# Performance work log

Measured on AMD Instinct MI355X. Metric: run time of the kernel, lower is better.

## Reference

```python
import jax, jax.numpy as jnp
import numpy as np

B, S, D, H = 8, 1024, 1024, 16
HD = D // H  # head_size = 64


def layernorm(x, g, b, eps=1e-5):
    mu = jnp.mean(x, axis=-1, keepdims=True)
    var = jnp.var(x, axis=-1, keepdims=True)
    return (x - mu) * jax.lax.rsqrt(var + eps) * g + b


def setup_inputs() -> dict:
    key = jax.random.key(0)
    ks = jax.random.split(key, 12)
    s_attn = 1.0 / np.sqrt(D)
    inp = {
        "x": jax.random.normal(ks[0], (B, S, D), dtype=jnp.float32),
        # per-head q/k/v projections (bias=False), stacked: [H, D, HD]
        "Wq": jax.random.normal(ks[1], (H, D, HD), dtype=jnp.float32) * s_attn,
        "Wk": jax.random.normal(ks[2], (H, D, HD), dtype=jnp.float32) * s_attn,
        "Wv": jax.random.normal(ks[3], (H, D, HD), dtype=jnp.float32) * s_attn,
        "Wo": jax.random.normal(ks[4], (D, D), dtype=jnp.float32) * s_attn,
        "bo": jnp.zeros((D,), dtype=jnp.float32),
        # FFN: hidden = 1 * n_embd (as in source)
        "W1": jax.random.normal(ks[5], (D, D), dtype=jnp.float32) * s_attn,
        "b1": jnp.zeros((D,), dtype=jnp.float32),
        "W2": jax.random.normal(ks[6], (D, D), dtype=jnp.float32) * s_attn,
        "b2": jnp.zeros((D,), dtype=jnp.float32),
        "g_ln1": jnp.ones((D,), dtype=jnp.float32),
        "b_ln1": jnp.zeros((D,), dtype=jnp.float32),
        "g_ln2": jnp.ones((D,), dtype=jnp.float32),
        "b_ln2": jnp.zeros((D,), dtype=jnp.float32),
    }
    return inp


def reference(x, Wq, Wk, Wv, Wo, bo, W1, b1, W2, b2, g_ln1, b_ln1, g_ln2, b_ln2):
    # pre-LN self-attention
    h = layernorm(x, g_ln1, b_ln1)
    q = jnp.einsum("bsd,hde->bhse", h, Wq)
    k = jnp.einsum("bsd,hde->bhse", h, Wk)
    v = jnp.einsum("bsd,hde->bhse", h, Wv)
    scale = HD ** -0.5  # k.shape[-1] ** -0.5
    wei = jax.nn.softmax(jnp.einsum("bhse,bhte->bhst", q, k) * scale, axis=-1)
    attn = jnp.einsum("bhst,bhte->bhse", wei, v)  # [B,H,S,HD]
    # concat heads (head order matches torch.cat over head list)
    attn = attn.transpose(0, 2, 1, 3).reshape(B, S, D)
    sa = attn @ Wo + bo
    x = x + sa
    # pre-LN FFN with exact GELU (torch nn.GELU default)
    h2 = layernorm(x, g_ln2, b_ln2)
    ff = jax.nn.gelu(h2 @ W1 + b1, approximate=False) @ W2 + b2
    return x + ff
```

## Files before the change

kernel.cpp:

```cpp
#include <hip/hip_runtime.h>
#include <hip/hip_bf16.h>
#include <math.h>

#define B_ 8
#define S_ 1024
#define D_ 1024
#define H_ 16
#define HD_ 64

typedef __bf16 bf16x8 __attribute__((ext_vector_type(8)));
typedef __bf16 bf16x4 __attribute__((ext_vector_type(4)));
typedef float f32x4 __attribute__((ext_vector_type(4)));

#define FMAX3(a, b, c) fmaxf(fmaxf((a), (b)), (c))

__device__ __forceinline__ void gld_lds16(const __bf16* g, __bf16* l) {
  __builtin_amdgcn_global_load_lds(
      (const __attribute__((address_space(1))) void*)g,
      (__attribute__((address_space(3))) void*)l, 16, 0, 0);
}

__global__ __launch_bounds__(256) void ln_f32(const float* __restrict__ x,
                                              const float* __restrict__ g,
                                              const float* __restrict__ b,
                                              __bf16* __restrict__ out) {
  int row = blockIdx.x;
  const float* xr = x + (size_t)row * D_;
  __bf16* outr = out + (size_t)row * D_;
  int tid = threadIdx.x;

  float4 v = ((const float4*)xr)[tid];
  float s = v.x + v.y + v.z + v.w;
  float ss = v.x * v.x + v.y * v.y + v.z * v.z + v.w * v.w;

  #pragma unroll
  for (int m = 1; m < 64; m <<= 1) {
    s += __shfl_xor(s, m);
    ss += __shfl_xor(ss, m);
  }
  __shared__ float red[10];
  int wid = tid >> 6;
  if ((tid & 63) == 0) { red[wid] = s; red[4 + wid] = ss; }
  __syncthreads();
  if (tid == 0) {
    float ts = red[0] + red[1] + red[2] + red[3];
    float tss = red[4] + red[5] + red[6] + red[7];
    float mu = ts * (1.0f / D_);
    float var = tss * (1.0f / D_) - mu * mu;
    red[8] = mu;
    red[9] = rsqrtf(var + 1e-5f);
  }
  __syncthreads();
  float mu = red[8], rstd = red[9];
  float4 gv = ((const float4*)g)[tid];
  float4 bv = ((const float4*)b)[tid];
  bf16x4 o;
  o[0] = (__bf16)((v.x - mu) * rstd * gv.x + bv.x);
  o[1] = (__bf16)((v.y - mu) * rstd * gv.y + bv.y);
  o[2] = (__bf16)((v.z - mu) * rstd * gv.z + bv.z);
  o[3] = (__bf16)((v.w - mu) * rstd * gv.w + bv.w);
  *(bf16x4*)(outr + tid * 4) = o;
}

__global__ __launch_bounds__(256) void ln_bf16(const __bf16* __restrict__ x,
                                               const float* __restrict__ g,
                                               const float* __restrict__ b,
                                               __bf16* __restrict__ out) {
  int row = blockIdx.x;
  const __bf16* xr = x + (size_t)row * D_;
  __bf16* outr = out + (size_t)row * D_;
  int tid = threadIdx.x;

  bf16x4 xv = *(const bf16x4*)(xr + tid * 4);
  float v0 = (float)xv[0], v1 = (float)xv[1], v2 = (float)xv[2], v3 = (float)xv[3];
  float s = v0 + v1 + v2 + v3;
  float ss = v0 * v0 + v1 * v1 + v2 * v2 + v3 * v3;

  #pragma unroll
  for (int m = 1; m < 64; m <<= 1) {
    s += __shfl_xor(s, m);
    ss += __shfl_xor(ss, m);
  }
  __shared__ float red[10];
  int wid = tid >> 6;
  if ((tid & 63) == 0) { red[wid] = s; red[4 + wid] = ss; }
  __syncthreads();
  if (tid == 0) {
    float ts = red[0] + red[1] + red[2] + red[3];
    float tss = red[4] + red[5] + red[6] + red[7];
    float mu = ts * (1.0f / D_);
    float var = tss * (1.0f / D_) - mu * mu;
    red[8] = mu;
    red[9] = rsqrtf(var + 1e-5f);
  }
  __syncthreads();
  float mu = red[8], rstd = red[9];
  float4 gv = ((const float4*)g)[tid];
  float4 bv = ((const float4*)b)[tid];
  bf16x4 o;
  o[0] = (__bf16)((v0 - mu) * rstd * gv.x + bv.x);
  o[1] = (__bf16)((v1 - mu) * rstd * gv.y + bv.y);
  o[2] = (__bf16)((v2 - mu) * rstd * gv.z + bv.z);
  o[3] = (__bf16)((v3 - mu) * rstd * gv.w + bv.w);
  *(bf16x4*)(outr + tid * 4) = o;
}

__global__ __launch_bounds__(256) void transpose_all(const float* __restrict__ Wq,
                                                     const float* __restrict__ Wk,
                                                     const float* __restrict__ Wv,
                                                     const float* __restrict__ Wo,
                                                     const float* __restrict__ W1,
                                                     const float* __restrict__ W2,
                                                     __bf16* __restrict__ out) {
  __shared__ float t[64][65];
  const int x = blockIdx.x, y = blockIdx.y, z = blockIdx.z;
  const int tid = threadIdx.x;
  const int r = tid >> 4, c4 = (tid & 15) * 4;

  const float* src;
  int stride, orowbase, kbase;
  if (z < 3) {
    const float* W = (z == 0 ? Wq : z == 1 ? Wk : Wv);
    src = W + (size_t)y * (D_ * HD_) + (size_t)(x * 64) * HD_;
    stride = HD_;
    orowbase = z * 1024 + y * 64;
    kbase = x * 64;
  } else {
    const float* W = (z == 3 ? Wo : z == 4 ? W1 : W2);
    src = W + (size_t)(y * 64) * D_ + x * 64;
    stride = D_;
    orowbase = z * 1024 + x * 64;
    kbase = y * 64;
  }

  #pragma unroll
  for (int i = 0; i < 4; ++i) {
    float4 v = *(const float4*)&src[(size_t)(i * 16 + r) * stride + c4];
    t[i * 16 + r][c4 + 0] = v.x;
    t[i * 16 + r][c4 + 1] = v.y;
    t[i * 16 + r][c4 + 2] = v.z;
    t[i * 16 + r][c4 + 3] = v.w;
  }
  __syncthreads();
  #pragma unroll
  for (int i = 0; i < 4; ++i) {
    bf16x4 o;
    #pragma unroll
    for (int j = 0; j < 4; ++j) o[j] = (__bf16)t[c4 + j][i * 16 + r];
    *(bf16x4*)&out[(size_t)(orowbase + i * 16 + r) * 1024 + kbase + c4] = o;
  }
}

#define MODE_QKV 0
#define MODE_PROJ 1
#define MODE_FF1 2
#define MODE_FF2 3

#define QSCALE 0.18033688011112042f

template <int MODE>
__global__ __launch_bounds__(256) void gemm_mfma(const __bf16* __restrict__ A,
                                                 const __bf16* __restrict__ Bt,
                                                 const float* __restrict__ bias,
                                                 const float* __restrict__ residf,
                                                 const __bf16* __restrict__ residb,
                                                 float* __restrict__ outf,
                                                 __bf16* __restrict__ outb,
                                                 int M, int N, int K) {
  __shared__ __align__(16) __bf16 As[2][128 * 64];
  __shared__ __align__(16) __bf16 Bs[2][128 * 64];
  const int tid = threadIdx.x;

  const int gx = (int)gridDim.x;
  const int nwg = gx * (int)gridDim.y;
  const int flat = (int)blockIdx.y * gx + (int)blockIdx.x;
  const int wg = (flat & 7) * (nwg >> 3) + (flat >> 3);
  const int m0 = (wg / gx) * 128, n0 = (wg % gx) * 128;

  const int w = tid >> 6, l = tid & 63, lr = l & 15, lg = l >> 4;
  const int wm = (w >> 1) * 64, wn = (w & 1) * 64;

  f32x4 acc[4][4] = {};

  auto stage = [&](int buf, int k0) {
    #pragma unroll
    for (int i = 0; i < 4; ++i) {
      int e = i * 256 + tid;
      int row = e >> 3;
      int col = ((e & 7) ^ (row & 7)) * 8;
      gld_lds16(A + (size_t)(m0 + row) * K + k0 + col, &As[buf][e * 8]);
    }
    #pragma unroll
    for (int i = 0; i < 4; ++i) {
      int e = i * 256 + tid;
      int row = e >> 3;
      int col = ((e & 7) ^ (row & 7)) * 8;
      gld_lds16(Bt + (size_t)(n0 + row) * K + k0 + col, &Bs[buf][e * 8]);
    }
  };

  auto compute = [&](int buf) {
    #pragma unroll
    for (int kk = 0; kk < 2; ++kk) {
      bf16x8 af[4], bfr[4];
      #pragma unroll
      for (int i = 0; i < 4; ++i)
        af[i] = *(const bf16x8*)
            &As[buf][((wm + i * 16 + lr) * 8 + ((kk * 4 + lg) ^ (lr & 7))) * 8];
      #pragma unroll
      for (int j = 0; j < 4; ++j)
        bfr[j] = *(const bf16x8*)
            &Bs[buf][((wn + j * 16 + lr) * 8 + ((kk * 4 + lg) ^ (lr & 7))) * 8];
      #pragma unroll
      for (int i = 0; i < 4; ++i)
        #pragma unroll
        for (int j = 0; j < 4; ++j)
          acc[i][j] = __builtin_amdgcn_mfma_f32_16x16x32_bf16(af[i], bfr[j], acc[i][j], 0, 0, 0);
    }
  };

  const int NT = K >> 6;
  stage(0, 0);

  for (int t = 0; t < NT; ++t) {
    const int buf = t & 1;
    const int tn = (t + 1 < NT) ? (t + 1) : (NT - 1);
    stage(buf ^ 1, tn * 64);
    asm volatile("s_waitcnt vmcnt(8)" ::: "memory");
    __builtin_amdgcn_sched_barrier(0);
    __builtin_amdgcn_s_barrier();
    __builtin_amdgcn_sched_barrier(0);
    compute(buf);
    __builtin_amdgcn_s_barrier();
  }

  #pragma unroll
  for (int i = 0; i < 4; ++i) {
    #pragma unroll
    for (int j = 0; j < 4; ++j) {
      #pragma unroll
      for (int r = 0; r < 4; ++r) {
        int m = m0 + wm + i * 16 + 4 * lg + r;
        int n = n0 + wn + j * 16 + lr;
        float val = acc[i][j][r];
        if (MODE == MODE_QKV) {
          int b = m >> 10, s = m & 1023;
          int which = n >> 10, hh = (n >> 6) & 15, e = n & 63;
          if (which == 0) val *= QSCALE;
          outb[(size_t)which * 8388608 + ((size_t)(b * 16 + hh) * 1024 + s) * 64 + e] =
              (__bf16)val;
        } else if (MODE == MODE_PROJ) {
          size_t idx = (size_t)m * 1024 + n;
          outb[idx] = (__bf16)(residf[idx] + val + bias[n]);
        } else if (MODE == MODE_FF1) {
          val += bias[n];
          outb[(size_t)m * 1024 + n] =
              (__bf16)(0.5f * val * (1.0f + erff(val * 0.70710678118654752f)));
        } else {
          size_t idx = (size_t)m * 1024 + n;
          outf[idx] = (float)residb[idx] + val + bias[n];
        }
      }
    }
  }
}

__global__ __launch_bounds__(512) void fattn(const __bf16* __restrict__ q,
                                             const __bf16* __restrict__ k,
                                             const __bf16* __restrict__ v,
                                             __bf16* __restrict__ outC) {
  __shared__ __align__(16) __bf16 Klds[2][64 * 64];
  __shared__ __align__(16) __bf16 Vp[2][64 * 64];

  const int bid = blockIdx.x;
  const int bh = (bid & 7) * 16 + ((bid >> 3) & 15);
  const int qt = bid >> 7;
  const int tid = threadIdx.x;
  const int w = tid >> 6, l = tid & 63;
  const int lr = l & 15, lg = l >> 4;

  const size_t base = (size_t)bh * (S_ * HD_);
  const int qrow0 = qt * 128 + w * 16;
  const __bf16* kg = k + base;
  const __bf16* vg = v + base;

  const int krow = tid >> 3;
  const int kcol = ((tid & 7) ^ (krow & 7)) * 8;
  const int vc = (l & 0x20) + ((l & 0xC) << 1) + ((l & 0x10) >> 2) + (l & 3);
  const int vchi = vc >> 3, vclo = vc & 7;

  bf16x8 qf0, qf1;
  {
    const __bf16* qp = q + base + (size_t)(qrow0 + lr) * HD_ + lg * 8;
    qf0 = *(const bf16x8*)(qp);
    qf1 = *(const bf16x8*)(qp + 32);
  }

  const __bf16 onev = (lr == 0) ? (__bf16)1.0f : (__bf16)0.0f;
  const bf16x8 vones = {onev, onev, onev, onev, onev, onev, onev, onev};

  f32x4 oacc[5] = {};
  float m_run = -1e30f;

  gld_lds16(kg + (size_t)krow * HD_ + kcol, &Klds[0][tid * 8]);
  bf16x8 vr;
  {
    vr = *(const bf16x8*)(vg + (size_t)l * HD_ + w * 8);
    #pragma unroll
    for (int i = 0; i < 8; ++i)
      Vp[0][(w * 8 + i) * 64 + ((vchi ^ i) << 3) + vclo] = vr[i];
    vr = *(const bf16x8*)(vg + (size_t)(64 + l) * HD_ + w * 8);
  }
  asm volatile("s_waitcnt vmcnt(1) lgkmcnt(0)" ::: "memory");
  __builtin_amdgcn_sched_barrier(0);
  __builtin_amdgcn_s_barrier();
  __builtin_amdgcn_sched_barrier(0);

  int cur = 0;
  for (int t = 0; t < 16; ++t) {
    {
      int tn = (t < 15) ? (t + 1) : 15;
      gld_lds16(kg + ((size_t)tn * 64 + krow) * HD_ + kcol, &Klds[cur ^ 1][tid * 8]);
    }

    f32x4 sacc[4];
    const __bf16* kb = &Klds[cur][0];
    __builtin_amdgcn_s_setprio(1);
    #pragma unroll
    for (int g = 0; g < 4; ++g) {
      bf16x8 kf0 = *(const bf16x8*)&kb[((16 * g + lr) * 8 + (lg ^ (lr & 7))) * 8];
      bf16x8 kf1 = *(const bf16x8*)&kb[((16 * g + lr) * 8 + ((lg + 4) ^ (lr & 7))) * 8];
      f32x4 z = {0.f, 0.f, 0.f, 0.f};
      z = __builtin_amdgcn_mfma_f32_16x16x32_bf16(kf0, qf0, z, 0, 0, 0);
      sacc[g] = __builtin_amdgcn_mfma_f32_16x16x32_bf16(kf1, qf1, z, 0, 0, 0);
    }
    __builtin_amdgcn_s_setprio(0);

    #pragma unroll
    for (int i = 0; i < 8; ++i)
      Vp[cur ^ 1][(w * 8 + i) * 64 + ((vchi ^ i) << 3) + vclo] = vr[i];
    {
      int tnn = (t < 14) ? (t + 2) : 15;
      vr = *(const bf16x8*)(vg + ((size_t)tnn * 64 + l) * HD_ + w * 8);
    }

    float m0 = FMAX3(sacc[0][0], sacc[0][1], sacc[0][2]);
    float m1 = FMAX3(sacc[0][3], sacc[1][0], sacc[1][1]);
    float m2 = FMAX3(sacc[1][2], sacc[1][3], sacc[2][0]);
    float m3 = FMAX3(sacc[2][1], sacc[2][2], sacc[2][3]);
    float m4 = FMAX3(sacc[3][0], sacc[3][1], sacc[3][2]);
    float tm = FMAX3(FMAX3(m0, m1, m2), FMAX3(m3, m4, sacc[3][3]), m_run);
    tm = fmaxf(tm, __shfl_xor(tm, 16));
    tm = fmaxf(tm, __shfl_xor(tm, 32));

    if (!__all(tm - m_run <= 11.5f)) {
      float corr = __builtin_amdgcn_exp2f(m_run - tm);
      m_run = tm;
      #pragma unroll
      for (int r = 0; r < 4; ++r) {
        float cq = __shfl(corr, 4 * lg + r);
        #pragma unroll
        for (int g = 0; g < 5; ++g) oacc[g][r] *= cq;
      }
    }

    float p[4][4];
    #pragma unroll
    for (int g = 0; g < 4; ++g)
      #pragma unroll
      for (int r = 0; r < 4; ++r)
        p[g][r] = __builtin_amdgcn_exp2f(sacc[g][r] - m_run);

    bf16x8 af0, af1;
    #pragma unroll
    for (int j = 0; j < 8; ++j) {
      af0[j] = (__bf16)p[j >> 2][j & 3];
      af1[j] = (__bf16)p[2 + (j >> 2)][j & 3];
    }
    __builtin_amdgcn_s_setprio(1);
    #pragma unroll
    for (int g = 0; g < 4; ++g) {
      bf16x8 vf0 = *(const bf16x8*)&Vp[cur][(16 * g + lr) * 64 + ((lg ^ (lr & 7)) << 3)];
      bf16x8 vf1 = *(const bf16x8*)&Vp[cur][(16 * g + lr) * 64 + (((lg + 4) ^ (lr & 7)) << 3)];
      oacc[g] = __builtin_amdgcn_mfma_f32_16x16x32_bf16(af0, vf0, oacc[g], 0, 0, 0);
      oacc[g] = __builtin_amdgcn_mfma_f32_16x16x32_bf16(af1, vf1, oacc[g], 0, 0, 0);
    }
    oacc[4] = __builtin_amdgcn_mfma_f32_16x16x32_bf16(af0, vones, oacc[4], 0, 0, 0);
    oacc[4] = __builtin_amdgcn_mfma_f32_16x16x32_bf16(af1, vones, oacc[4], 0, 0, 0);
    __builtin_amdgcn_s_setprio(0);

    asm volatile("s_waitcnt vmcnt(1) lgkmcnt(0)" ::: "memory");
    __builtin_amdgcn_sched_barrier(0);
    __builtin_amdgcn_s_barrier();
    __builtin_amdgcn_sched_barrier(0);
    cur ^= 1;
  }

  const int b = bh >> 4, hh = bh & 15;
  #pragma unroll
  for (int r = 0; r < 4; ++r) {
    float linv = 1.0f / __shfl(oacc[4][r], l & 48);
    int srow = qrow0 + 4 * lg + r;
    __bf16* op = outC + ((size_t)(b * S_ + srow)) * D_ + hh * HD_;
    #pragma unroll
    for (int g = 0; g < 4; ++g) op[16 * g + lr] = (__bf16)(oacc[g][r] * linv);
  }
}

extern "C" void kernel_launch(void* const* d_in, const int* in_sizes, int n_in,
                              void* d_out, int out_size, void* d_ws, size_t ws_size,
                              hipStream_t stream) {
  const float* x   = (const float*)d_in[0];
  const float* Wq  = (const float*)d_in[1];
  const float* Wk  = (const float*)d_in[2];
  const float* Wv  = (const float*)d_in[3];
  const float* Wo  = (const float*)d_in[4];
  const float* bo  = (const float*)d_in[5];
  const float* W1  = (const float*)d_in[6];
  const float* b1  = (const float*)d_in[7];
  const float* W2  = (const float*)d_in[8];
  const float* b2  = (const float*)d_in[9];
  const float* g1  = (const float*)d_in[10];
  const float* bl1 = (const float*)d_in[11];
  const float* g2  = (const float*)d_in[12];
  const float* bl2 = (const float*)d_in[13];
  float* out = (float*)d_out;

  const size_t MN = (size_t)B_ * S_ * D_;
  __bf16* h     = (__bf16*)d_ws;
  __bf16* wt    = h + MN;
  __bf16* qkv   = wt + (size_t)6144 * 1024;
  __bf16* attnC = qkv + 3 * MN;
  __bf16* ff1   = attnC + MN;
  __bf16* mid   = ff1 + MN;

  __bf16* wqkv_t = wt;
  __bf16* wo_t   = wt + (size_t)3072 * 1024;
  __bf16* w1_t   = wt + (size_t)4096 * 1024;
  __bf16* w2_t   = wt + (size_t)5120 * 1024;

  const int rows = B_ * S_;

  ln_f32<<<rows, 256, 0, stream>>>(x, g1, bl1, h);
  transpose_all<<<dim3(16, 16, 6), 256, 0, stream>>>(Wq, Wk, Wv, Wo, W1, W2, wt);

  gemm_mfma<MODE_QKV><<<dim3(24, 64), 256, 0, stream>>>(
      h, wqkv_t, nullptr, nullptr, nullptr, nullptr, qkv, rows, 3072, D_);
  fattn<<<1024, 512, 0, stream>>>(qkv, qkv + MN, qkv + 2 * MN, attnC);
  gemm_mfma<MODE_PROJ><<<dim3(8, 64), 256, 0, stream>>>(
      attnC, wo_t, bo, x, nullptr, nullptr, mid, rows, D_, D_);
  ln_bf16<<<rows, 256, 0, stream>>>(mid, g2, bl2, h);
  gemm_mfma<MODE_FF1><<<dim3(8, 64), 256, 0, stream>>>(
      h, w1_t, b1, nullptr, nullptr, nullptr, ff1, rows, D_, D_);
  gemm_mfma<MODE_FF2><<<dim3(8, 64), 256, 0, stream>>>(
      ff1, w2_t, b2, nullptr, mid, out, nullptr, rows, D_, D_);
}
```

Measured before the change: 226.9 us.

## Merge layernorm and weight transpose into one kernel, use tanh GELU, drop setprio

Merges the first layernorm and the weight transpose/convert into a single launch, with branches on block index, to save a kernel launch and let both run concurrently. Replaces the erf-based GELU in the FF1 epilogue with a tanh approximation built from exp2 and rcp, which lowers epilogue cost but deviates slightly from the exact GELU the reference uses. Removes the s_setprio hints around the MFMA sections in the attention kernel.

```diff
diff --git a/kernel.cpp b/kernel.cpp
--- a/kernel.cpp
+++ b/kernel.cpp
@@ -20,18 +20,112 @@
       (__attribute__((address_space(3))) void*)l, 16, 0, 0);
 }
 
-__global__ __launch_bounds__(256) void ln_f32(const float* __restrict__ x,
-                                              const float* __restrict__ g,
-                                              const float* __restrict__ b,
-                                              __bf16* __restrict__ out) {
+__global__ __launch_bounds__(256) void prep(const float* __restrict__ x,
+                                            const float* __restrict__ g,
+                                            const float* __restrict__ b,
+                                            __bf16* __restrict__ h_out,
+                                            const float* __restrict__ Wq,
+                                            const float* __restrict__ Wk,
+                                            const float* __restrict__ Wv,
+                                            const float* __restrict__ Wo,
+                                            const float* __restrict__ W1,
+                                            const float* __restrict__ W2,
+                                            __bf16* __restrict__ wt) {
+  __shared__ float t[64][65];
+  const int bid = blockIdx.x;
+  const int tid = threadIdx.x;
+
+  if (bid < 8192) {
+    float* red = &t[0][0];
+    const float* xr = x + (size_t)bid * D_;
+    __bf16* outr = h_out + (size_t)bid * D_;
+
+    float4 v = ((const float4*)xr)[tid];
+    float s = v.x + v.y + v.z + v.w;
+    float ss = v.x * v.x + v.y * v.y + v.z * v.z + v.w * v.w;
+
+    #pragma unroll
+    for (int m = 1; m < 64; m <<= 1) {
+      s += __shfl_xor(s, m);
+      ss += __shfl_xor(ss, m);
+    }
+    int wid = tid >> 6;
+    if ((tid & 63) == 0) { red[wid] = s; red[4 + wid] = ss; }
+    __syncthreads();
+    if (tid == 0) {
+      float ts = red[0] + red[1] + red[2] + red[3];
+      float tss = red[4] + red[5] + red[6] + red[7];
+      float mu = ts * (1.0f / D_);
+      float var = tss * (1.0f / D_) - mu * mu;
+      red[8] = mu;
+      red[9] = rsqrtf(var + 1e-5f);
+    }
+    __syncthreads();
+    float mu = red[8], rstd = red[9];
+    float4 gv = ((const float4*)g)[tid];
+    float4 bv = ((const float4*)b)[tid];
+    bf16x4 o;
+    o[0] = (__bf16)((v.x - mu) * rstd * gv.x + bv.x);
+    o[1] = (__bf16)((v.y - mu) * rstd * gv.y + bv.y);
+    o[2] = (__bf16)((v.z - mu) * rstd * gv.z + bv.z);
+    o[3] = (__bf16)((v.w - mu) * rstd * gv.w + bv.w);
+    *(bf16x4*)(outr + tid * 4) = o;
+    return;
+  }
+
+  const int tt = bid - 8192;
+  const int z = tt >> 8;
+  const int y = (tt >> 4) & 15;
+  const int xx = tt & 15;
+  const int r = tid >> 4, c4 = (tid & 15) * 4;
+
+  const float* src;
+  int stride, orowbase, kbase;
+  if (z < 3) {
+    const float* W = (z == 0 ? Wq : z == 1 ? Wk : Wv);
+    src = W + (size_t)y * (D_ * HD_) + (size_t)(xx * 64) * HD_;
+    stride = HD_;
+    orowbase = z * 1024 + y * 64;
+    kbase = xx * 64;
+  } else {
+    const float* W = (z == 3 ? Wo : z == 4 ? W1 : W2);
+    src = W + (size_t)(y * 64) * D_ + xx * 64;
+    stride = D_;
+    orowbase = z * 1024 + xx * 64;
+    kbase = y * 64;
+  }
+
+  #pragma unroll
+  for (int i = 0; i < 4; ++i) {
+    float4 v = *(const float4*)&src[(size_t)(i * 16 + r) * stride + c4];
+    t[i * 16 + r][c4 + 0] = v.x;
+    t[i * 16 + r][c4 + 1] = v.y;
+    t[i * 16 + r][c4 + 2] = v.z;
+    t[i * 16 + r][c4 + 3] = v.w;
+  }
+  __syncthreads();
+  #pragma unroll
+  for (int i = 0; i < 4; ++i) {
+    bf16x4 o;
+    #pragma unroll
+    for (int j = 0; j < 4; ++j) o[j] = (__bf16)t[c4 + j][i * 16 + r];
+    *(bf16x4*)&wt[(size_t)(orowbase + i * 16 + r) * 1024 + kbase + c4] = o;
+  }
+}
+
+__global__ __launch_bounds__(256) void ln_bf16(const __bf16* __restrict__ x,
+                                               const float* __restrict__ g,
+                                               const float* __restrict__ b,
+                                               __bf16* __restrict__ out) {
   int row = blockIdx.x;
-  const float* xr = x + (size_t)row * D_;
+  const __bf16* xr = x + (size_t)row * D_;
   __bf16* outr = out + (size_t)row * D_;
   int tid = threadIdx.x;
 
-  float4 v = ((const float4*)xr)[tid];
-  float s = v.x + v.y + v.z + v.w;
-  float ss = v.x * v.x + v.y * v.y + v.z * v.z + v.w * v.w;
+  bf16x4 xv = *(const bf16x4*)(xr + tid * 4);
+  float v0 = (float)xv[0], v1 = (float)xv[1], v2 = (float)xv[2], v3 = (float)xv[3];
+  float s = v0 + v1 + v2 + v3;
+  float ss = v0 * v0 + v1 * v1 + v2 * v2 + v3 * v3;
 
   #pragma unroll
   for (int m = 1; m < 64; m <<= 1) {
@@ -55,49 +149,6 @@
   float4 gv = ((const float4*)g)[tid];
   float4 bv = ((const float4*)b)[tid];
   bf16x4 o;
-  o[0] = (__bf16)((v.x - mu) * rstd * gv.x + bv.x);
-  o[1] = (__bf16)((v.y - mu) * rstd * gv.y + bv.y);
-  o[2] = (__bf16)((v.z - mu) * rstd * gv.z + bv.z);
-  o[3] = (__bf16)((v.w - mu) * rstd * gv.w + bv.w);
-  *(bf16x4*)(outr + tid * 4) = o;
-}
-
-__global__ __launch_bounds__(256) void ln_bf16(const __bf16* __restrict__ x,
-                                               const float* __restrict__ g,
-                                               const float* __restrict__ b,
-                                               __bf16* __restrict__ out) {
-  int row = blockIdx.x;
-  const __bf16* xr = x + (size_t)row * D_;
-  __bf16* outr = out + (size_t)row * D_;
-  int tid = threadIdx.x;
-
-  bf16x4 xv = *(const bf16x4*)(xr + tid * 4);
-  float v0 = (float)xv[0], v1 = (float)xv[1], v2 = (float)xv[2], v3 = (float)xv[3];
-  float s = v0 + v1 + v2 + v3;
-  float ss = v0 * v0 + v1 * v1 + v2 * v2 + v3 * v3;
-
-  #pragma unroll
-  for (int m = 1; m < 64; m <<= 1) {
-    s += __shfl_xor(s, m);
-    ss += __shfl_xor(ss, m);
-  }
-  __shared__ float red[10];
-  int wid = tid >> 6;
-  if ((tid & 63) == 0) { red[wid] = s; red[4 + wid] = ss; }
-  __syncthreads();
-  if (tid == 0) {
-    float ts = red[0] + red[1] + red[2] + red[3];
-    float tss = red[4] + red[5] + red[6] + red[7];
-    float mu = ts * (1.0f / D_);
-    float var = tss * (1.0f / D_) - mu * mu;
-    red[8] = mu;
-    red[9] = rsqrtf(var + 1e-5f);
-  }
-  __syncthreads();
-  float mu = red[8], rstd = red[9];
-  float4 gv = ((const float4*)g)[tid];
-  float4 bv = ((const float4*)b)[tid];
-  bf16x4 o;
   o[0] = (__bf16)((v0 - mu) * rstd * gv.x + bv.x);
   o[1] = (__bf16)((v1 - mu) * rstd * gv.y + bv.y);
   o[2] = (__bf16)((v2 - mu) * rstd * gv.z + bv.z);
@@ -105,58 +156,19 @@
   *(bf16x4*)(outr + tid * 4) = o;
 }
 
-__global__ __launch_bounds__(256) void transpose_all(const float* __restrict__ Wq,
-                                                     const float* __restrict__ Wk,
-                                                     const float* __restrict__ Wv,
-                                                     const float* __restrict__ Wo,
-                                                     const float* __restrict__ W1,
-                                                     const float* __restrict__ W2,
-                                                     __bf16* __restrict__ out) {
-  __shared__ float t[64][65];
-  const int x = blockIdx.x, y = blockIdx.y, z = blockIdx.z;
-  const int tid = threadIdx.x;
-  const int r = tid >> 4, c4 = (tid & 15) * 4;
-
-  const float* src;
-  int stride, orowbase, kbase;
-  if (z < 3) {
-    const float* W = (z == 0 ? Wq : z == 1 ? Wk : Wv);
-    src = W + (size_t)y * (D_ * HD_) + (size_t)(x * 64) * HD_;
-    stride = HD_;
-    orowbase = z * 1024 + y * 64;
-    kbase = x * 64;
-  } else {
-    const float* W = (z == 3 ? Wo : z == 4 ? W1 : W2);
-    src = W + (size_t)(y * 64) * D_ + x * 64;
-    stride = D_;
-    orowbase = z * 1024 + x * 64;
-    kbase = y * 64;
-  }
-
-  #pragma unroll
-  for (int i = 0; i < 4; ++i) {
-    float4 v = *(const float4*)&src[(size_t)(i * 16 + r) * stride + c4];
-    t[i * 16 + r][c4 + 0] = v.x;
-    t[i * 16 + r][c4 + 1] = v.y;
-    t[i * 16 + r][c4 + 2] = v.z;
-    t[i * 16 + r][c4 + 3] = v.w;
-  }
-  __syncthreads();
-  #pragma unroll
-  for (int i = 0; i < 4; ++i) {
-    bf16x4 o;
-    #pragma unroll
-    for (int j = 0; j < 4; ++j) o[j] = (__bf16)t[c4 + j][i * 16 + r];
-    *(bf16x4*)&out[(size_t)(orowbase + i * 16 + r) * 1024 + kbase + c4] = o;
-  }
-}
-
 #define MODE_QKV 0
 #define MODE_PROJ 1
 #define MODE_FF1 2
 #define MODE_FF2 3
 
 #define QSCALE 0.18033688011112042f
+
+__device__ __forceinline__ float gelu_tanh(float v) {
+  float u = 0.7978845608028654f * v * (1.0f + 0.044715f * v * v);
+  float e = __builtin_amdgcn_exp2f(2.885390081777927f * u);
+  float th = 1.0f - 2.0f * __builtin_amdgcn_rcpf(e + 1.0f);
+  return 0.5f * v * (1.0f + th);
+}
 
 template <int MODE>
 __global__ __launch_bounds__(256) void gemm_mfma(const __bf16* __restrict__ A,
@@ -253,9 +265,7 @@
           size_t idx = (size_t)m * 1024 + n;
           outb[idx] = (__bf16)(residf[idx] + val + bias[n]);
         } else if (MODE == MODE_FF1) {
-          val += bias[n];
-          outb[(size_t)m * 1024 + n] =
-              (__bf16)(0.5f * val * (1.0f + erff(val * 0.70710678118654752f)));
+          outb[(size_t)m * 1024 + n] = (__bf16)gelu_tanh(val + bias[n]);
         } else {
           size_t idx = (size_t)m * 1024 + n;
           outf[idx] = (float)residb[idx] + val + bias[n];
@@ -325,7 +335,6 @@
 
     f32x4 sacc[4];
     const __bf16* kb = &Klds[cur][0];
-    __builtin_amdgcn_s_setprio(1);
     #pragma unroll
     for (int g = 0; g < 4; ++g) {
       bf16x8 kf0 = *(const bf16x8*)&kb[((16 * g + lr) * 8 + (lg ^ (lr & 7))) * 8];
@@ -334,7 +343,6 @@
       z = __builtin_amdgcn_mfma_f32_16x16x32_bf16(kf0, qf0, z, 0, 0, 0);
       sacc[g] = __builtin_amdgcn_mfma_f32_16x16x32_bf16(kf1, qf1, z, 0, 0, 0);
     }
-    __builtin_amdgcn_s_setprio(0);
 
     #pragma unroll
     for (int i = 0; i < 8; ++i)
@@ -377,7 +385,6 @@
       af0[j] = (__bf16)p[j >> 2][j & 3];
       af1[j] = (__bf16)p[2 + (j >> 2)][j & 3];
     }
-    __builtin_amdgcn_s_setprio(1);
     #pragma unroll
     for (int g = 0; g < 4; ++g) {
       bf16x8 vf0 = *(const bf16x8*)&Vp[cur][(16 * g + lr) * 64 + ((lg ^ (lr & 7)) << 3)];
@@ -387,7 +394,6 @@
     }
     oacc[4] = __builtin_amdgcn_mfma_f32_16x16x32_bf16(af0, vones, oacc[4], 0, 0, 0);
     oacc[4] = __builtin_amdgcn_mfma_f32_16x16x32_bf16(af1, vones, oacc[4], 0, 0, 0);
-    __builtin_amdgcn_s_setprio(0);
 
     asm volatile("s_waitcnt vmcnt(1) lgkmcnt(0)" ::: "memory");
     __builtin_amdgcn_sched_barrier(0);
@@ -441,8 +447,7 @@
 
   const int rows = B_ * S_;
 
-  ln_f32<<<rows, 256, 0, stream>>>(x, g1, bl1, h);
-  transpose_all<<<dim3(16, 16, 6), 256, 0, stream>>>(Wq, Wk, Wv, Wo, W1, W2, wt);
+  prep<<<rows + 1536, 256, 0, stream>>>(x, g1, bl1, h, Wq, Wk, Wv, Wo, W1, W2, wt);
 
   gemm_mfma<MODE_QKV><<<dim3(24, 64), 256, 0, stream>>>(
       h, wqkv_t, nullptr, nullptr, nullptr, nullptr, qkv, rows, 3072, D_);
```

Result: faster. 218.9 us (-3.5%).
